# Kernel optimization log

Measured on AMD Instinct MI355X. Metric: run time of the kernel, lower is better.

The kernel has to match this reference:

```python
import jax, jax.numpy as jnp
import numpy as np

N = 50000      # nodes
E = 600000     # edges (before self-loops)
F_IN = 128     # input features
H = 128        # hidden width
C = 64         # classes
NEG_SLOPE = 0.2


def setup_inputs() -> dict:
    key = jax.random.key(0)
    ks = jax.random.split(key, 16)
    x = jax.random.normal(ks[0], (N, F_IN), dtype=jnp.float32)
    edge_index = jax.random.randint(ks[1], (2, E), 0, N, dtype=jnp.int32)
    dims = [(F_IN, H), (H, H), (H, C)]
    inp = {"x": x, "edge_index": edge_index}
    for l, (din, dout) in enumerate(dims):
        kw, ka, kb = jax.random.split(ks[2 + l], 3)
        scale = 1.0 / np.sqrt(din)
        inp[f"W{l}"] = jax.random.normal(kw, (din, dout), dtype=jnp.float32) * scale
        inp[f"a_src{l}"] = jax.random.normal(ka, (dout,), dtype=jnp.float32) * 0.1
        inp[f"a_dst{l}"] = jax.random.normal(kb, (dout,), dtype=jnp.float32) * 0.1
        inp[f"b{l}"] = jnp.zeros((dout,), dtype=jnp.float32)
    return inp


def gat_conv(x, src, dst, W, a_s, a_d, b):
    n = x.shape[0]
    h = x @ W                                   # [n, dout]
    alpha = jax.nn.leaky_relu((h @ a_s)[src] + (h @ a_d)[dst], NEG_SLOPE)  # [e]
    # segment softmax over destination-node neighborhoods
    m = jax.ops.segment_max(alpha, dst, num_segments=n)
    ex = jnp.exp(alpha - m[dst])
    denom = jax.ops.segment_sum(ex, dst, num_segments=n)
    coef = ex / denom[dst]                      # [e]
    out = jax.ops.segment_sum(h[src] * coef[:, None], dst, num_segments=n)
    return out + b


def reference(x, edge_index, W0, a_src0, a_dst0, b0, W1, a_src1, a_dst1, b1, W2, a_src2, a_dst2, b2):
    n = x.shape[0]
    loops = jnp.arange(n, dtype=edge_index.dtype)   # add_self_loops=True (PyG default)
    src = jnp.concatenate([edge_index[0], loops])
    dst = jnp.concatenate([edge_index[1], loops])
    h = gat_conv(x, src, dst, W0, a_src0, a_dst0, b0)
    h = h * jax.nn.sigmoid(h)                        # SiLU between layers
    h = gat_conv(h, src, dst, W1, a_src1, a_dst1, b1)
    h = h * jax.nn.sigmoid(h)
    h = gat_conv(h, src, dst, W2, a_src2, a_dst2, b2)
    return jax.nn.log_softmax(h, axis=1)
```

## Files before the change

kernel.cpp:

```cpp
#include <hip/hip_runtime.h>
#include <math.h>

#define NEG_SLOPE 0.2f
constexpr int BS_SCAN = 1024;
constexpr int HB_MAX = 160;
constexpr int WPB    = 32;

typedef __attribute__((ext_vector_type(8))) short bfrag;
typedef __attribute__((ext_vector_type(4))) float f32x4;

__device__ __forceinline__ float lrelu(float x) { return x > 0.f ? x : NEG_SLOPE * x; }

__device__ __forceinline__ unsigned short f2bf(float f) {
    union { float f; unsigned u; } v; v.f = f;
    unsigned r = v.u + 0x7fffu + ((v.u >> 16) & 1u);
    return (unsigned short)(r >> 16);
}
__device__ __forceinline__ float bf2f_lo(unsigned p) { union { unsigned u; float f; } v; v.u = p << 16; return v.f; }
__device__ __forceinline__ float bf2f_hi(unsigned p) { union { unsigned u; float f; } v; v.u = p & 0xffff0000u; return v.f; }

__device__ __forceinline__ void wswz_body(const float* __restrict__ W, unsigned short* __restrict__ out,
                                          int DOUT, int tid) {
    int lane = tid & 63;
    int g = tid >> 6;
    int NT = DOUT >> 4;
    int tile = g % NT, kstep = g / NT;
    int q = lane >> 4, c = lane & 15;
    int n_ = tile * 16 + c;
    unsigned short v[8];
#pragma unroll
    for (int j = 0; j < 8; ++j) {
        int k = kstep * 32 + q * 8 + j;
        v[j] = f2bf(W[k * DOUT + n_]);
    }
    uint4 o;
    o.x = (unsigned)v[0] | ((unsigned)v[1] << 16);
    o.y = (unsigned)v[2] | ((unsigned)v[3] << 16);
    o.z = (unsigned)v[4] | ((unsigned)v[5] << 16);
    o.w = (unsigned)v[6] | ((unsigned)v[7] << 16);
    *(uint4*)(out + (size_t)tid * 8) = o;
}

__global__ __launch_bounds__(256) void histswz_kernel(
    const int* __restrict__ dstv, unsigned* __restrict__ hist32, unsigned char* __restrict__ rank8,
    int E, int hb, int nw,
    const float* __restrict__ W0, const float* __restrict__ W1, const float* __restrict__ W2,
    unsigned short* __restrict__ wz0, unsigned short* __restrict__ wz1, unsigned short* __restrict__ wz2)
{
    __shared__ unsigned bins[12544];
    int b = blockIdx.x;
    if (b >= hb) {
        int wb = b - hb;
        if (wb < 8)       wswz_body(W0, wz0, 128, wb * 256 + threadIdx.x);
        else if (wb < 16) wswz_body(W1, wz1, 128, (wb - 8) * 256 + threadIdx.x);
        else {
            int tid = (wb - 16) * 256 + threadIdx.x;
            if (tid < 1024) wswz_body(W2, wz2, 64, tid);
        }
        return;
    }
    int tid = threadIdx.x;
    for (int i = tid; i < nw; i += 256) bins[i] = 0u;
    __syncthreads();
    int base = b * 4096;
#pragma unroll
    for (int j = 0; j < 4; ++j) {
        int e0 = base + j * 1024 + tid * 4;
        if (e0 + 3 < E) {
            int4 d4 = *(const int4*)(dstv + e0);
            unsigned r0, r1, r2, r3;
            { int sh = (d4.x & 3) * 8; r0 = (atomicAdd(&bins[d4.x >> 2], 1u << sh) >> sh) & 0xffu; }
            { int sh = (d4.y & 3) * 8; r1 = (atomicAdd(&bins[d4.y >> 2], 1u << sh) >> sh) & 0xffu; }
            { int sh = (d4.z & 3) * 8; r2 = (atomicAdd(&bins[d4.z >> 2], 1u << sh) >> sh) & 0xffu; }
            { int sh = (d4.w & 3) * 8; r3 = (atomicAdd(&bins[d4.w >> 2], 1u << sh) >> sh) & 0xffu; }
            *(unsigned*)(rank8 + e0) = r0 | (r1 << 8) | (r2 << 16) | (r3 << 24);
        } else {
            for (int k = 0; k < 4; ++k) {
                int e = e0 + k;
                if (e < E) {
                    int d = dstv[e];
                    int sh = (d & 3) * 8;
                    rank8[e] = (unsigned char)((atomicAdd(&bins[d >> 2], 1u << sh) >> sh) & 0xffu);
                }
            }
        }
    }
    __syncthreads();
    unsigned* hrow = hist32 + (size_t)b * nw;
    for (int i = tid; i < nw; i += 256) hrow[i] = bins[i];
}

__global__ __launch_bounds__(1024) void scan1_kernel(const int* __restrict__ counts,
                                                     int* __restrict__ excl,
                                                     int* __restrict__ totals, int n) {
    __shared__ int sm[BS_SCAN];
    int tid = threadIdx.x;
    int i = blockIdx.x * BS_SCAN + tid;
    int v = (i < n) ? counts[i] : 0;
    int val = v;
    sm[tid] = val;
    for (int off = 1; off < BS_SCAN; off <<= 1) {
        __syncthreads();
        int t = (tid >= off) ? sm[tid - off] : 0;
        __syncthreads();
        val += t; sm[tid] = val;
    }
    if (i < n) excl[i] = val - v;
    if (tid == BS_SCAN - 1) totals[blockIdx.x] = val;
}

__global__ __launch_bounds__(1024) void scan23_kernel(int* __restrict__ row_ptr,
                                                      const int* __restrict__ totals,
                                                      int n, int E, int nb) {
    __shared__ int s_off;
    int tid = threadIdx.x;
    if (tid < 64) {
        int v = (tid < blockIdx.x && tid < nb) ? totals[tid] : 0;
#pragma unroll
        for (int off = 32; off; off >>= 1) v += __shfl_xor(v, off);
        if (tid == 0) s_off = v;
    }
    __syncthreads();
    int off = s_off;
    int i = blockIdx.x * BS_SCAN + tid;
    if (i < n) row_ptr[i] += off;
    if (i == 0) row_ptr[n] = E;
}

template<int DOUT, bool ABF>
__device__ __forceinline__ void gemm_body(
    int bid, const void* __restrict__ Xv, const unsigned short* __restrict__ Wswz,
    const float* __restrict__ avs, const float* __restrict__ avd,
    unsigned* __restrict__ Hout, float* __restrict__ as_out, float* __restrict__ ad_out,
    int n, float* __restrict__ smemw)
{
    constexpr int NT = DOUT / 16;
    constexpr int NCH = NT / 4;
    int lane = threadIdx.x & 63;
    int w = threadIdx.x >> 6;
    int q = lane >> 4, c = lane & 15;
    int rowbase = bid * 64 + w * 16;
    int arow = rowbase + c;

    f32x4 acc[NT];
#pragma unroll
    for (int t = 0; t < NT; ++t) acc[t] = (f32x4){0.f, 0.f, 0.f, 0.f};

#pragma unroll
    for (int ks = 0; ks < 4; ++ks) {
        bfrag a = (bfrag)0;
        int k0 = ks * 32 + q * 8;
        if (ABF) {
            if (arow < n) a = *(const bfrag*)((const unsigned short*)Xv + (size_t)arow * 128 + k0);
        } else {
            if (arow < n) {
                const float* xp = (const float*)Xv + (size_t)arow * 128 + k0;
                float4 x0 = *(const float4*)xp, x1 = *(const float4*)(xp + 4);
                a[0] = (short)f2bf(x0.x); a[1] = (short)f2bf(x0.y);
                a[2] = (short)f2bf(x0.z); a[3] = (short)f2bf(x0.w);
                a[4] = (short)f2bf(x1.x); a[5] = (short)f2bf(x1.y);
                a[6] = (short)f2bf(x1.z); a[7] = (short)f2bf(x1.w);
            }
        }
#pragma unroll
        for (int t = 0; t < NT; ++t) {
            bfrag b = *(const bfrag*)(Wswz + ((size_t)(ks * NT + t) * 64 + lane) * 8);
            acc[t] = __builtin_amdgcn_mfma_f32_16x16x32_bf16(a, b, acc[t], 0, 0, 0);
        }
    }

    float* sm = smemw + w * (16 * 68);
    int dr = lane >> 2;
    int c0 = (lane & 3) * 16;
    float s = 0.f, d = 0.f;

#pragma unroll
    for (int ch = 0; ch < NCH; ++ch) {
        if (ch) {
            asm volatile("s_waitcnt lgkmcnt(0)" ::: "memory");
            __builtin_amdgcn_wave_barrier();
        }
#pragma unroll
        for (int t = 0; t < 4; ++t)
#pragma unroll
            for (int r = 0; r < 4; ++r)
                sm[(q * 4 + r) * 68 + t * 16 + c] = acc[ch * 4 + t][r];
        __builtin_amdgcn_wave_barrier();

#pragma unroll
        for (int it = 0; it < 4; ++it) {
            int r = it * 4 + q;
            int grow = rowbase + r;
            float4 v = *(const float4*)(sm + r * 68 + c * 4);
            uint2 o;
            o.x = (unsigned)f2bf(v.x) | ((unsigned)f2bf(v.y) << 16);
            o.y = (unsigned)f2bf(v.z) | ((unsigned)f2bf(v.w) << 16);
            if (grow < n) *(uint2*)(Hout + (size_t)grow * (DOUT / 2) + ch * 32 + c * 2) = o;
        }
#pragma unroll
        for (int j = 0; j < 16; j += 4) {
            float4 hv = *(const float4*)(sm + dr * 68 + c0 + j);
            float4 av = *(const float4*)(avs + ch * 64 + c0 + j);
            float4 dv = *(const float4*)(avd + ch * 64 + c0 + j);
            s += hv.x * av.x + hv.y * av.y + hv.z * av.z + hv.w * av.w;
            d += hv.x * dv.x + hv.y * dv.y + hv.z * dv.z + hv.w * dv.w;
        }
    }

    s += __shfl_down(s, 2); s += __shfl_down(s, 1);
    d += __shfl_down(d, 2); d += __shfl_down(d, 1);
    int grow = rowbase + dr;
    if ((lane & 3) == 0 && grow < n) { as_out[grow] = s; ad_out[grow] = d; }
}

__global__ __launch_bounds__(256) void scangemm0_kernel(
    const unsigned* __restrict__ hist32, unsigned* __restrict__ off32,
    int* __restrict__ counts, int hb, int nw, int sb,
    const float* __restrict__ X, const unsigned short* __restrict__ wz0,
    const float* __restrict__ avs, const float* __restrict__ avd,
    unsigned* __restrict__ Hout, float* __restrict__ as_out, float* __restrict__ ad_out, int n)
{
    __shared__ unsigned smem[HB_MAX * (WPB + 1)];
    int b = blockIdx.x;
    if (b < sb) {
        unsigned (*tile)[WPB + 1] = (unsigned (*)[WPB + 1])smem;
        int tid = threadIdx.x;
        int w0 = b * WPB;
        int wl = tid & 31;
        int w = w0 + wl;
        for (int r = tid >> 5; r < hb; r += 8)
            tile[r][wl] = (w < nw) ? hist32[(size_t)r * nw + w] : 0u;
        __syncthreads();
        if (tid < WPB) {
            unsigned run = 0;
            for (int r = 0; r < hb; ++r) {
                unsigned v = tile[r][tid];
                tile[r][tid] = run;
                run += v;
            }
            int ww = w0 + tid;
            if (ww < nw) {
                int i0 = ww * 4;
                int4 cv;
                cv.x = (int)(run & 0xffu);         cv.y = (int)((run >> 8) & 0xffu);
                cv.z = (int)((run >> 16) & 0xffu); cv.w = (int)((run >> 24) & 0xffu);
                if (i0 + 3 < n) *(int4*)(counts + i0) = cv;
                else {
                    if (i0 < n)     counts[i0]     = cv.x;
                    if (i0 + 1 < n) counts[i0 + 1] = cv.y;
                    if (i0 + 2 < n) counts[i0 + 2] = cv.z;
                    if (i0 + 3 < n) counts[i0 + 3] = cv.w;
                }
            }
        }
        __syncthreads();
        for (int r = tid >> 5; r < hb; r += 8)
            if (w < nw) off32[(size_t)r * nw + w] = tile[r][wl];
        return;
    }
    gemm_body<128, false>(b - sb, X, wz0, avs, avd, Hout, as_out, ad_out, n, (float*)smem);
}

template<int DOUT>
__global__ __launch_bounds__(256) void gemm_kernel(
    const unsigned* __restrict__ Xb, const unsigned short* __restrict__ Wswz,
    const float* __restrict__ avs, const float* __restrict__ avd,
    unsigned* __restrict__ Hout, float* __restrict__ as_out, float* __restrict__ ad_out, int n)
{
    __shared__ float smem[4 * 16 * 68];
    gemm_body<DOUT, true>(blockIdx.x, Xb, Wswz, avs, avd, Hout, as_out, ad_out, n, smem);
}

__global__ __launch_bounds__(256) void scatter_kernel(
    const int* __restrict__ ei, const unsigned char* __restrict__ rank8,
    const unsigned* __restrict__ off32, const int* __restrict__ row_ptr,
    unsigned short* __restrict__ col, int E, int nw)
{
    int e0 = (blockIdx.x * 256 + (int)threadIdx.x) * 4;
    if (e0 + 3 < E) {
        int4 s4 = *(const int4*)(ei + e0);
        int4 d4 = *(const int4*)(ei + E + e0);
        unsigned r4 = *(const unsigned*)(rank8 + e0);
        size_t bb = (size_t)(e0 >> 12) * nw;
        unsigned o0 = (off32[bb + (d4.x >> 2)] >> ((d4.x & 3) * 8)) & 0xffu;
        unsigned o1 = (off32[bb + (d4.y >> 2)] >> ((d4.y & 3) * 8)) & 0xffu;
        unsigned o2 = (off32[bb + (d4.z >> 2)] >> ((d4.z & 3) * 8)) & 0xffu;
        unsigned o3 = (off32[bb + (d4.w >> 2)] >> ((d4.w & 3) * 8)) & 0xffu;
        col[row_ptr[d4.x] + (int)o0 + (int)(r4 & 0xffu)]         = (unsigned short)s4.x;
        col[row_ptr[d4.y] + (int)o1 + (int)((r4 >> 8) & 0xffu)]  = (unsigned short)s4.y;
        col[row_ptr[d4.z] + (int)o2 + (int)((r4 >> 16) & 0xffu)] = (unsigned short)s4.z;
        col[row_ptr[d4.w] + (int)o3 + (int)((r4 >> 24) & 0xffu)] = (unsigned short)s4.w;
    } else {
        for (int k = 0; k < 4; ++k) {
            int e = e0 + k;
            if (e < E) {
                int d = ei[E + e];
                unsigned o = (off32[(size_t)(e >> 12) * nw + (d >> 2)] >> ((d & 3) * 8)) & 0xffu;
                col[row_ptr[d] + (int)o + (int)rank8[e]] = (unsigned short)ei[e];
            }
        }
    }
}

__global__ __launch_bounds__(256) void agg128_kernel(
    const unsigned* __restrict__ Hb, const float* __restrict__ as_v,
    const float* __restrict__ ad_v, const float* __restrict__ bias,
    const int* __restrict__ row_ptr, const unsigned short* __restrict__ col,
    unsigned* __restrict__ outb, int n)
{
    int lane = threadIdx.x & 63;
    int g = lane >> 4, i = lane & 15;
    int node = blockIdx.x * 16 + (threadIdx.x >> 6) * 4 + g;
    if (node >= n) return;
    int beg = row_ptr[node], end = row_ptr[node + 1];
    float adv = ad_v[node];
    float c_self = __expf(fminf(lrelu(as_v[node] + adv), 60.f));

    uint4 hs = *(const uint4*)(Hb + (size_t)node * 64 + i * 4);
    float acc[8];
    acc[0] = c_self * bf2f_lo(hs.x); acc[1] = c_self * bf2f_hi(hs.x);
    acc[2] = c_self * bf2f_lo(hs.y); acc[3] = c_self * bf2f_hi(hs.y);
    acc[4] = c_self * bf2f_lo(hs.z); acc[5] = c_self * bf2f_hi(hs.z);
    acc[6] = c_self * bf2f_lo(hs.w); acc[7] = c_self * bf2f_hi(hs.w);
    float dsum = (i == 0) ? c_self : 0.f;
    int lanebase = g * 16;

    for (int cb = beg; cb < end; cb += 16) {
        int idx = cb + i;
        int sreg = 0; float creg = 0.f;
        if (idx < end) {
            sreg = col[idx];
            creg = __expf(fminf(lrelu(as_v[sreg] + adv), 60.f));
        }
        dsum += creg;
        int cnt = end - cb; if (cnt > 16) cnt = 16;
        for (int k = 0; k < cnt; k += 4) {
            int s0 = __shfl(sreg, lanebase + k);
            int s1 = __shfl(sreg, lanebase + k + 1);
            int s2 = __shfl(sreg, lanebase + k + 2);
            int s3 = __shfl(sreg, lanebase + k + 3);
            float c0 = __shfl(creg, lanebase + k);
            float c1 = __shfl(creg, lanebase + k + 1);
            float c2 = __shfl(creg, lanebase + k + 2);
            float c3 = __shfl(creg, lanebase + k + 3);
            uint4 h0 = *(const uint4*)(Hb + (size_t)s0 * 64 + i * 4);
            uint4 h1 = *(const uint4*)(Hb + (size_t)s1 * 64 + i * 4);
            uint4 h2 = *(const uint4*)(Hb + (size_t)s2 * 64 + i * 4);
            uint4 h3 = *(const uint4*)(Hb + (size_t)s3 * 64 + i * 4);
            acc[0] += c0 * bf2f_lo(h0.x); acc[1] += c0 * bf2f_hi(h0.x);
            acc[2] += c0 * bf2f_lo(h0.y); acc[3] += c0 * bf2f_hi(h0.y);
            acc[4] += c0 * bf2f_lo(h0.z); acc[5] += c0 * bf2f_hi(h0.z);
            acc[6] += c0 * bf2f_lo(h0.w); acc[7] += c0 * bf2f_hi(h0.w);
            acc[0] += c1 * bf2f_lo(h1.x); acc[1] += c1 * bf2f_hi(h1.x);
            acc[2] += c1 * bf2f_lo(h1.y); acc[3] += c1 * bf2f_hi(h1.y);
            acc[4] += c1 * bf2f_lo(h1.z); acc[5] += c1 * bf2f_hi(h1.z);
            acc[6] += c1 * bf2f_lo(h1.w); acc[7] += c1 * bf2f_hi(h1.w);
            acc[0] += c2 * bf2f_lo(h2.x); acc[1] += c2 * bf2f_hi(h2.x);
            acc[2] += c2 * bf2f_lo(h2.y); acc[3] += c2 * bf2f_hi(h2.y);
            acc[4] += c2 * bf2f_lo(h2.z); acc[5] += c2 * bf2f_hi(h2.z);
            acc[6] += c2 * bf2f_lo(h2.w); acc[7] += c2 * bf2f_hi(h2.w);
            acc[0] += c3 * bf2f_lo(h3.x); acc[1] += c3 * bf2f_hi(h3.x);
            acc[2] += c3 * bf2f_lo(h3.y); acc[3] += c3 * bf2f_hi(h3.y);
            acc[4] += c3 * bf2f_lo(h3.z); acc[5] += c3 * bf2f_hi(h3.z);
            acc[6] += c3 * bf2f_lo(h3.w); acc[7] += c3 * bf2f_hi(h3.w);
        }
    }

#pragma unroll
    for (int off = 8; off; off >>= 1) dsum += __shfl_xor(dsum, off);
    float inv = 1.f / dsum;

    float4 b0v = *(const float4*)(bias + i * 8);
    float4 b1v = *(const float4*)(bias + i * 8 + 4);
    float v0 = acc[0] * inv + b0v.x, v1 = acc[1] * inv + b0v.y;
    float v2 = acc[2] * inv + b0v.z, v3 = acc[3] * inv + b0v.w;
    float v4 = acc[4] * inv + b1v.x, v5 = acc[5] * inv + b1v.y;
    float v6 = acc[6] * inv + b1v.z, v7 = acc[7] * inv + b1v.w;
    v0 /= (1.f + __expf(-v0)); v1 /= (1.f + __expf(-v1));
    v2 /= (1.f + __expf(-v2)); v3 /= (1.f + __expf(-v3));
    v4 /= (1.f + __expf(-v4)); v5 /= (1.f + __expf(-v5));
    v6 /= (1.f + __expf(-v6)); v7 /= (1.f + __expf(-v7));
    uint4 o;
    o.x = (unsigned)f2bf(v0) | ((unsigned)f2bf(v1) << 16);
    o.y = (unsigned)f2bf(v2) | ((unsigned)f2bf(v3) << 16);
    o.z = (unsigned)f2bf(v4) | ((unsigned)f2bf(v5) << 16);
    o.w = (unsigned)f2bf(v6) | ((unsigned)f2bf(v7) << 16);
    *(uint4*)(outb + (size_t)node * 64 + i * 4) = o;
}

__global__ __launch_bounds__(256) void agg64_kernel(
    const unsigned* __restrict__ Hb, const float* __restrict__ as_v,
    const float* __restrict__ ad_v, const float* __restrict__ bias,
    const int* __restrict__ row_ptr, const unsigned short* __restrict__ col,
    float* __restrict__ out, int n)
{
    int lane = threadIdx.x & 63;
    int g = lane >> 4, i = lane & 15;
    int node = blockIdx.x * 16 + (threadIdx.x >> 6) * 4 + g;
    if (node >= n) return;
    int beg = row_ptr[node], end = row_ptr[node + 1];
    float adv = ad_v[node];
    float c_self = __expf(fminf(lrelu(as_v[node] + adv), 60.f));

    uint2 hs = *(const uint2*)(Hb + (size_t)node * 32 + i * 2);
    float acc[4];
    acc[0] = c_self * bf2f_lo(hs.x); acc[1] = c_self * bf2f_hi(hs.x);
    acc[2] = c_self * bf2f_lo(hs.y); acc[3] = c_self * bf2f_hi(hs.y);
    float dsum = (i == 0) ? c_self : 0.f;
    int lanebase = g * 16;

    for (int cb = beg; cb < end; cb += 16) {
        int idx = cb + i;
        int sreg = 0; float creg = 0.f;
        if (idx < end) {
            sreg = col[idx];
            creg = __expf(fminf(lrelu(as_v[sreg] + adv), 60.f));
        }
        dsum += creg;
        int cnt = end - cb; if (cnt > 16) cnt = 16;
        for (int k = 0; k < cnt; k += 4) {
            int s0 = __shfl(sreg, lanebase + k);
            int s1 = __shfl(sreg, lanebase + k + 1);
            int s2 = __shfl(sreg, lanebase + k + 2);
            int s3 = __shfl(sreg, lanebase + k + 3);
            float c0 = __shfl(creg, lanebase + k);
            float c1 = __shfl(creg, lanebase + k + 1);
            float c2 = __shfl(creg, lanebase + k + 2);
            float c3 = __shfl(creg, lanebase + k + 3);
            uint2 h0 = *(const uint2*)(Hb + (size_t)s0 * 32 + i * 2);
            uint2 h1 = *(const uint2*)(Hb + (size_t)s1 * 32 + i * 2);
            uint2 h2 = *(const uint2*)(Hb + (size_t)s2 * 32 + i * 2);
            uint2 h3 = *(const uint2*)(Hb + (size_t)s3 * 32 + i * 2);
            acc[0] += c0 * bf2f_lo(h0.x); acc[1] += c0 * bf2f_hi(h0.x);
            acc[2] += c0 * bf2f_lo(h0.y); acc[3] += c0 * bf2f_hi(h0.y);
            acc[0] += c1 * bf2f_lo(h1.x); acc[1] += c1 * bf2f_hi(h1.x);
            acc[2] += c1 * bf2f_lo(h1.y); acc[3] += c1 * bf2f_hi(h1.y);
            acc[0] += c2 * bf2f_lo(h2.x); acc[1] += c2 * bf2f_hi(h2.x);
            acc[2] += c2 * bf2f_lo(h2.y); acc[3] += c2 * bf2f_hi(h2.y);
            acc[0] += c3 * bf2f_lo(h3.x); acc[1] += c3 * bf2f_hi(h3.x);
            acc[2] += c3 * bf2f_lo(h3.y); acc[3] += c3 * bf2f_hi(h3.y);
        }
    }

#pragma unroll
    for (int off = 8; off; off >>= 1) dsum += __shfl_xor(dsum, off);
    float inv = 1.f / dsum;

    float4 bv = *(const float4*)(bias + i * 4);
    float v0 = acc[0] * inv + bv.x, v1 = acc[1] * inv + bv.y;
    float v2 = acc[2] * inv + bv.z, v3 = acc[3] * inv + bv.w;
    float mx = fmaxf(fmaxf(v0, v1), fmaxf(v2, v3));
#pragma unroll
    for (int off = 8; off; off >>= 1) mx = fmaxf(mx, __shfl_xor(mx, off));
    float sum = __expf(v0 - mx) + __expf(v1 - mx) + __expf(v2 - mx) + __expf(v3 - mx);
#pragma unroll
    for (int off = 8; off; off >>= 1) sum += __shfl_xor(sum, off);
    float ls = mx + logf(sum);
    float4 o = make_float4(v0 - ls, v1 - ls, v2 - ls, v3 - ls);
    *(float4*)(out + (size_t)node * 64 + i * 4) = o;
}

extern "C" void kernel_launch(void* const* d_in, const int* in_sizes, int n_in,
                              void* d_out, int out_size, void* d_ws, size_t ws_size,
                              hipStream_t stream) {
    const float* x   = (const float*)d_in[0];
    const int*   ei  = (const int*)d_in[1];
    const float* W0  = (const float*)d_in[2];
    const float* as0 = (const float*)d_in[3];
    const float* ad0 = (const float*)d_in[4];
    const float* b0  = (const float*)d_in[5];
    const float* W1  = (const float*)d_in[6];
    const float* as1 = (const float*)d_in[7];
    const float* ad1 = (const float*)d_in[8];
    const float* b1  = (const float*)d_in[9];
    const float* W2  = (const float*)d_in[10];
    const float* as2 = (const float*)d_in[11];
    const float* ad2 = (const float*)d_in[12];
    const float* b2  = (const float*)d_in[13];

    int n = in_sizes[0] / 128;
    int E = in_sizes[1] / 2;
    const int* dstv = ei + E;

    int hb = (E + 4095) >> 12;
    int nw = (n + 3) >> 2;

    char* wsp = (char*)d_ws;
    auto alloc = [&](size_t bytes) {
        char* p = wsp;
        wsp += (bytes + 255) & ~(size_t)255;
        return p;
    };
    int*   counts  = (int*)alloc((size_t)n * 4);
    int*   row_ptr = (int*)alloc((size_t)(n + 1) * 4);
    int*   totals  = (int*)alloc(256 * 4);
    unsigned* hist32 = (unsigned*)alloc((size_t)hb * nw * 4);
    unsigned* off32  = (unsigned*)alloc((size_t)hb * nw * 4);
    unsigned char* rank8 = (unsigned char*)alloc((size_t)E);
    unsigned short* col = (unsigned short*)alloc((size_t)E * 2);
    unsigned short* wz0 = (unsigned short*)alloc(128 * 128 * 2);
    unsigned short* wz1 = (unsigned short*)alloc(128 * 128 * 2);
    unsigned short* wz2 = (unsigned short*)alloc(128 * 64 * 2);
    unsigned* hb0  = (unsigned*)alloc((size_t)n * 64 * 4);
    unsigned* hb1  = (unsigned*)alloc((size_t)n * 64 * 4);
    unsigned* hf   = (unsigned*)alloc((size_t)n * 32 * 4);
    unsigned* xb   = (unsigned*)alloc((size_t)n * 64 * 4);
    float*    asbA = (float*)alloc((size_t)n * 4);
    float*    adbA = (float*)alloc((size_t)n * 4);
    float*    asbB = (float*)alloc((size_t)n * 4);
    float*    adbB = (float*)alloc((size_t)n * 4);

    int gemmb = (n + 63) / 64;
    int nodeb = (n + 15) / 16;
    int nb  = (n + BS_SCAN - 1) / BS_SCAN;
    int sb  = (nw + WPB - 1) / WPB;
    int scb = (E + 1023) / 1024;

    histswz_kernel<<<hb + 20, 256, 0, stream>>>(dstv, hist32, rank8, E, hb, nw,
                                                W0, W1, W2, wz0, wz1, wz2);
    scangemm0_kernel<<<sb + gemmb, 256, 0, stream>>>(hist32, off32, counts, hb, nw, sb,
                                                     x, wz0, as0, ad0, hb0, asbA, adbA, n);
    scan1_kernel<<<nb, BS_SCAN, 0, stream>>>(counts, row_ptr, totals, n);
    scan23_kernel<<<nb, BS_SCAN, 0, stream>>>(row_ptr, totals, n, E, nb);
    scatter_kernel<<<scb, 256, 0, stream>>>(ei, rank8, off32, row_ptr, col, E, nw);
    agg128_kernel<<<nodeb, 256, 0, stream>>>(hb0, asbA, adbA, b0, row_ptr, col, xb, n);
    gemm_kernel<128><<<gemmb, 256, 0, stream>>>(xb, wz1, as1, ad1, hb1, asbB, adbB, n);
    agg128_kernel<<<nodeb, 256, 0, stream>>>(hb1, asbB, adbB, b1, row_ptr, col, xb, n);
    gemm_kernel<64><<<gemmb, 256, 0, stream>>>(xb, wz2, as2, ad2, hf, asbA, adbA, n);
    agg64_kernel<<<nodeb, 256, 0, stream>>>(hf, asbA, adbA, b2, row_ptr, col, (float*)d_out, n);
}
```

Baseline: 227.6 us.

## Fuse scan and scatter into one kernel with spin barriers; degree-sort aggregation nodes

Replaces the two scan kernels and the scatter kernel with a single csrfinish kernel. Its blocks coordinate through global atomic counters and spin-wait in place of separate launches, which removes two launch boundaries. The same kernel builds a degree-bucketed permutation of nodes, and the aggregation kernels now process nodes in that order so the four nodes sharing a wavefront have similar neighbour counts. Histogram zeroing and copy-out are vectorised to uint4. The spin-waits assume every producer block can be resident at once, which risks deadlock if they cannot. The permutation also makes aggregation reads of H and writes of the output less contiguous.

```diff
diff --git a/kernel.cpp b/kernel.cpp
--- a/kernel.cpp
+++ b/kernel.cpp
@@ -43,7 +43,7 @@
 
 __global__ __launch_bounds__(256) void histswz_kernel(
     const int* __restrict__ dstv, unsigned* __restrict__ hist32, unsigned char* __restrict__ rank8,
-    int E, int hb, int nw,
+    int E, int hb, int nw, int* __restrict__ done,
     const float* __restrict__ W0, const float* __restrict__ W1, const float* __restrict__ W2,
     unsigned short* __restrict__ wz0, unsigned short* __restrict__ wz1, unsigned short* __restrict__ wz2)
 {
@@ -51,6 +51,7 @@
     int b = blockIdx.x;
     if (b >= hb) {
         int wb = b - hb;
+        if (wb == 0 && threadIdx.x == 0) { done[0] = 0; done[1] = 0; }
         if (wb < 8)       wswz_body(W0, wz0, 128, wb * 256 + threadIdx.x);
         else if (wb < 16) wswz_body(W1, wz1, 128, (wb - 8) * 256 + threadIdx.x);
         else {
@@ -60,7 +61,15 @@
         return;
     }
     int tid = threadIdx.x;
-    for (int i = tid; i < nw; i += 256) bins[i] = 0u;
+    int nw4 = nw >> 2;
+    bool v4ok = (nw & 3) == 0;
+    if (v4ok) {
+        uint4 z4; z4.x = z4.y = z4.z = z4.w = 0u;
+        uint4* b4 = (uint4*)bins;
+        for (int i = tid; i < nw4; i += 256) b4[i] = z4;
+    } else {
+        for (int i = tid; i < nw; i += 256) bins[i] = 0u;
+    }
     __syncthreads();
     int base = b * 4096;
 #pragma unroll
@@ -87,44 +96,13 @@
     }
     __syncthreads();
     unsigned* hrow = hist32 + (size_t)b * nw;
-    for (int i = tid; i < nw; i += 256) hrow[i] = bins[i];
-}
-
-__global__ __launch_bounds__(1024) void scan1_kernel(const int* __restrict__ counts,
-                                                     int* __restrict__ excl,
-                                                     int* __restrict__ totals, int n) {
-    __shared__ int sm[BS_SCAN];
-    int tid = threadIdx.x;
-    int i = blockIdx.x * BS_SCAN + tid;
-    int v = (i < n) ? counts[i] : 0;
-    int val = v;
-    sm[tid] = val;
-    for (int off = 1; off < BS_SCAN; off <<= 1) {
-        __syncthreads();
-        int t = (tid >= off) ? sm[tid - off] : 0;
-        __syncthreads();
-        val += t; sm[tid] = val;
-    }
-    if (i < n) excl[i] = val - v;
-    if (tid == BS_SCAN - 1) totals[blockIdx.x] = val;
-}
-
-__global__ __launch_bounds__(1024) void scan23_kernel(int* __restrict__ row_ptr,
-                                                      const int* __restrict__ totals,
-                                                      int n, int E, int nb) {
-    __shared__ int s_off;
-    int tid = threadIdx.x;
-    if (tid < 64) {
-        int v = (tid < blockIdx.x && tid < nb) ? totals[tid] : 0;
-#pragma unroll
-        for (int off = 32; off; off >>= 1) v += __shfl_xor(v, off);
-        if (tid == 0) s_off = v;
-    }
-    __syncthreads();
-    int off = s_off;
-    int i = blockIdx.x * BS_SCAN + tid;
-    if (i < n) row_ptr[i] += off;
-    if (i == 0) row_ptr[n] = E;
+    if (v4ok) {
+        uint4* h4 = (uint4*)hrow;
+        const uint4* s4 = (const uint4*)bins;
+        for (int i = tid; i < nw4; i += 256) h4[i] = s4[i];
+    } else {
+        for (int i = tid; i < nw; i += 256) hrow[i] = bins[i];
+    }
 }
 
 template<int DOUT, bool ABF>
@@ -261,22 +239,81 @@
     gemm_body<128, false>(b - sb, X, wz0, avs, avd, Hout, as_out, ad_out, n, (float*)smem);
 }
 
-template<int DOUT>
-__global__ __launch_bounds__(256) void gemm_kernel(
-    const unsigned* __restrict__ Xb, const unsigned short* __restrict__ Wswz,
-    const float* __restrict__ avs, const float* __restrict__ avd,
-    unsigned* __restrict__ Hout, float* __restrict__ as_out, float* __restrict__ ad_out, int n)
-{
-    __shared__ float smem[4 * 16 * 68];
-    gemm_body<DOUT, true>(blockIdx.x, Xb, Wswz, avs, avd, Hout, as_out, ad_out, n, smem);
-}
-
-__global__ __launch_bounds__(256) void scatter_kernel(
+__global__ __launch_bounds__(1024) void csrfinish_kernel(
+    const int* __restrict__ counts, int* __restrict__ row_ptr,
+    int* __restrict__ totals, int* __restrict__ done, int* __restrict__ perm,
     const int* __restrict__ ei, const unsigned char* __restrict__ rank8,
-    const unsigned* __restrict__ off32, const int* __restrict__ row_ptr,
-    unsigned short* __restrict__ col, int E, int nw)
-{
-    int e0 = (blockIdx.x * 256 + (int)threadIdx.x) * 4;
+    const unsigned* __restrict__ off32, unsigned short* __restrict__ col,
+    int n, int E, int nb, int nw)
+{
+    __shared__ int sm[BS_SCAN];
+    __shared__ int s_off;
+    int tid = threadIdx.x;
+    int b = blockIdx.x;
+
+    if (b < nb) {
+        int i = b * BS_SCAN + tid;
+        int v = (i < n) ? counts[i] : 0;
+        int val = v;
+        sm[tid] = val;
+        for (int off = 1; off < BS_SCAN; off <<= 1) {
+            __syncthreads();
+            int t = (tid >= off) ? sm[tid - off] : 0;
+            __syncthreads();
+            val += t; sm[tid] = val;
+        }
+        if (tid == BS_SCAN - 1) {
+            totals[b] = val;
+            __threadfence();
+            atomicAdd(&done[0], 1);
+        }
+        if (tid < 64) {
+            while (atomicAdd(&done[0], 0) < nb) {}
+            __threadfence();
+            int t = (tid < b && tid < nb) ? totals[tid] : 0;
+#pragma unroll
+            for (int off = 32; off; off >>= 1) t += __shfl_xor(t, off);
+            if (tid == 0) s_off = t;
+        }
+        __syncthreads();
+        if (i < n) row_ptr[i] = val - v + s_off;
+        if (i == 0) row_ptr[n] = E;
+        __syncthreads();
+        if (tid == 0) {
+            __threadfence();
+            atomicAdd(&done[1], 1);
+        }
+        return;
+    }
+
+    if (b == nb) {
+        __shared__ int bh[32];
+        if (tid < 32) bh[tid] = 0;
+        __syncthreads();
+        for (int i = tid; i < n; i += 1024) {
+            int k = counts[i]; k = k > 31 ? 31 : k;
+            atomicAdd(&bh[k], 1);
+        }
+        __syncthreads();
+        if (tid == 0) {
+            int run = 0;
+            for (int k = 0; k < 32; ++k) { int t = bh[k]; bh[k] = run; run += t; }
+        }
+        __syncthreads();
+        for (int i = tid; i < n; i += 1024) {
+            int k = counts[i]; k = k > 31 ? 31 : k;
+            int pos = atomicAdd(&bh[k], 1);
+            perm[pos] = i;
+        }
+        return;
+    }
+
+    if (tid == 0) {
+        while (atomicAdd(&done[1], 0) < nb) {}
+        __threadfence();
+    }
+    __syncthreads();
+    int e0 = (b - nb - 1) * 4096 + tid * 4;
     if (e0 + 3 < E) {
         int4 s4 = *(const int4*)(ei + e0);
         int4 d4 = *(const int4*)(ei + E + e0);
@@ -302,16 +339,27 @@
     }
 }
 
+template<int DOUT>
+__global__ __launch_bounds__(256) void gemm_kernel(
+    const unsigned* __restrict__ Xb, const unsigned short* __restrict__ Wswz,
+    const float* __restrict__ avs, const float* __restrict__ avd,
+    unsigned* __restrict__ Hout, float* __restrict__ as_out, float* __restrict__ ad_out, int n)
+{
+    __shared__ float smem[4 * 16 * 68];
+    gemm_body<DOUT, true>(blockIdx.x, Xb, Wswz, avs, avd, Hout, as_out, ad_out, n, smem);
+}
+
 __global__ __launch_bounds__(256) void agg128_kernel(
     const unsigned* __restrict__ Hb, const float* __restrict__ as_v,
     const float* __restrict__ ad_v, const float* __restrict__ bias,
     const int* __restrict__ row_ptr, const unsigned short* __restrict__ col,
-    unsigned* __restrict__ outb, int n)
+    const int* __restrict__ perm, unsigned* __restrict__ outb, int n)
 {
     int lane = threadIdx.x & 63;
     int g = lane >> 4, i = lane & 15;
-    int node = blockIdx.x * 16 + (threadIdx.x >> 6) * 4 + g;
-    if (node >= n) return;
+    int raw = blockIdx.x * 16 + (threadIdx.x >> 6) * 4 + g;
+    if (raw >= n) return;
+    int node = perm[raw];
     int beg = row_ptr[node], end = row_ptr[node + 1];
     float adv = ad_v[node];
     float c_self = __expf(fminf(lrelu(as_v[node] + adv), 60.f));
@@ -392,12 +440,13 @@
     const unsigned* __restrict__ Hb, const float* __restrict__ as_v,
     const float* __restrict__ ad_v, const float* __restrict__ bias,
     const int* __restrict__ row_ptr, const unsigned short* __restrict__ col,
-    float* __restrict__ out, int n)
+    const int* __restrict__ perm, float* __restrict__ out, int n)
 {
     int lane = threadIdx.x & 63;
     int g = lane >> 4, i = lane & 15;
-    int node = blockIdx.x * 16 + (threadIdx.x >> 6) * 4 + g;
-    if (node >= n) return;
+    int raw = blockIdx.x * 16 + (threadIdx.x >> 6) * 4 + g;
+    if (raw >= n) return;
+    int node = perm[raw];
     int beg = row_ptr[node], end = row_ptr[node + 1];
     float adv = ad_v[node];
     float c_self = __expf(fminf(lrelu(as_v[node] + adv), 60.f));
@@ -493,7 +542,9 @@
     };
     int*   counts  = (int*)alloc((size_t)n * 4);
     int*   row_ptr = (int*)alloc((size_t)(n + 1) * 4);
+    int*   perm    = (int*)alloc((size_t)n * 4);
     int*   totals  = (int*)alloc(256 * 4);
+    int*   done    = (int*)alloc(256);
     unsigned* hist32 = (unsigned*)alloc((size_t)hb * nw * 4);
     unsigned* off32  = (unsigned*)alloc((size_t)hb * nw * 4);
     unsigned char* rank8 = (unsigned char*)alloc((size_t)E);
@@ -514,18 +565,17 @@
     int nodeb = (n + 15) / 16;
     int nb  = (n + BS_SCAN - 1) / BS_SCAN;
     int sb  = (nw + WPB - 1) / WPB;
-    int scb = (E + 1023) / 1024;
-
-    histswz_kernel<<<hb + 20, 256, 0, stream>>>(dstv, hist32, rank8, E, hb, nw,
+    int scb = (E + 4095) / 4096;
+
+    histswz_kernel<<<hb + 20, 256, 0, stream>>>(dstv, hist32, rank8, E, hb, nw, done,
                                                 W0, W1, W2, wz0, wz1, wz2);
     scangemm0_kernel<<<sb + gemmb, 256, 0, stream>>>(hist32, off32, counts, hb, nw, sb,
                                                      x, wz0, as0, ad0, hb0, asbA, adbA, n);
-    scan1_kernel<<<nb, BS_SCAN, 0, stream>>>(counts, row_ptr, totals, n);
-    scan23_kernel<<<nb, BS_SCAN, 0, stream>>>(row_ptr, totals, n, E, nb);
-    scatter_kernel<<<scb, 256, 0, stream>>>(ei, rank8, off32, row_ptr, col, E, nw);
-    agg128_kernel<<<nodeb, 256, 0, stream>>>(hb0, asbA, adbA, b0, row_ptr, col, xb, n);
+    csrfinish_kernel<<<nb + 1 + scb, 1024, 0, stream>>>(counts, row_ptr, totals, done, perm,
+                                                        ei, rank8, off32, col, n, E, nb, nw);
+    agg128_kernel<<<nodeb, 256, 0, stream>>>(hb0, asbA, adbA, b0, row_ptr, col, perm, xb, n);
     gemm_kernel<128><<<gemmb, 256, 0, stream>>>(xb, wz1, as1, ad1, hb1, asbB, adbB, n);
-    agg128_kernel<<<nodeb, 256, 0, stream>>>(hb1, asbB, adbB, b1, row_ptr, col, xb, n);
+    agg128_kernel<<<nodeb, 256, 0, stream>>>(hb1, asbB, adbB, b1, row_ptr, col, perm, xb, n);
     gemm_kernel<64><<<gemmb, 256, 0, stream>>>(xb, wz2, as2, ad2, hf, asbA, adbA, n);
-    agg64_kernel<<<nodeb, 256, 0, stream>>>(hf, asbA, adbA, b2, row_ptr, col, (float*)d_out, n);
-}
+    agg64_kernel<<<nodeb, 256, 0, stream>>>(hf, asbA, adbA, b2, row_ptr, col, perm, (float*)d_out, n);
+}
```

New measurement: 245.9 us. 1.08x slower.
